# Optimization experiments

Measured on AMD Instinct MI355X. Metric: run time of the kernel, lower is better.

## Reference

```python
import jax, jax.numpy as jnp
import numpy as np

N_NODES = 50000
N_EDGES = 1250000
D = 64


def setup_inputs() -> dict:
    key = jax.random.key(0)
    ks = jax.random.split(key, 9)
    s = 1.0 / np.sqrt(D)
    return {
        "y": jax.random.normal(ks[0], (N_NODES, D), dtype=jnp.float32),
        "src": jax.random.randint(ks[1], (N_EDGES,), 0, N_NODES, dtype=jnp.int32),
        "dst": jax.random.randint(ks[2], (N_EDGES,), 0, N_NODES, dtype=jnp.int32),
        "W1": jax.random.normal(ks[3], (D, D), dtype=jnp.float32) * s,
        "b1": jnp.zeros((D,), dtype=jnp.float32),
        "W2": jax.random.normal(ks[4], (D, D), dtype=jnp.float32) * s,
        "b2": jnp.zeros((D,), dtype=jnp.float32),
        "U1": jax.random.normal(ks[5], (D, D), dtype=jnp.float32) * s,
        "c1": jnp.zeros((D,), dtype=jnp.float32),
        "U2": jax.random.normal(ks[6], (D, D), dtype=jnp.float32) * s,
        "c2": jnp.zeros((D,), dtype=jnp.float32),
    }


def reference(y, src, dst, W1, b1, W2, b2, U1, c1, U2, c2):
    # msg = relu(FNN_pre(y[src])) ; FNN = Linear -> ReLU -> Linear
    xs = y[src]                                        # [E, D] gather
    h1 = jax.nn.relu(xs @ W1 + b1)                     # [E, D]
    msg = jax.nn.relu(h1 @ W2 + b2)                    # [E, D]
    # z = segment-sum of messages at destination nodes
    z = jax.ops.segment_sum(msg, dst, num_segments=N_NODES)  # [N, D]
    # h = relu(FNN_update(z))
    h2 = jax.nn.relu(z @ U1 + c1)                      # [N, D]
    h = jax.nn.relu(h2 @ U2 + c2)                      # [N, D]
    return h
```

## Files before the change

### kernel.cpp

```cpp
#include <hip/hip_runtime.h>

#define D 64
#define CHUNK 4096
#define BSHIFT 8
#define CAP 8192

typedef unsigned int uint;
typedef unsigned short ushort;

using bf16x8 = __attribute__((ext_vector_type(8))) short;
using f32x4  = __attribute__((ext_vector_type(4))) float;

__device__ __forceinline__ uint f2bf(float f) {
    uint u = __float_as_uint(f);
    return (u + 0x7fffu + ((u >> 16) & 1u)) >> 16;
}
__device__ __forceinline__ uint pk2(float a, float b) {
    return f2bf(a) | (f2bf(b) << 16);
}

#define ACC8M(v, aE, aO, mk) do {                                              \
    aE[0] = fmaf(mk, __uint_as_float((v).x << 16), aE[0]);                     \
    aO[0] = fmaf(mk, __uint_as_float((v).x & 0xffff0000u), aO[0]);             \
    aE[1] = fmaf(mk, __uint_as_float((v).y << 16), aE[1]);                     \
    aO[1] = fmaf(mk, __uint_as_float((v).y & 0xffff0000u), aO[1]);             \
    aE[2] = fmaf(mk, __uint_as_float((v).z << 16), aE[2]);                     \
    aO[2] = fmaf(mk, __uint_as_float((v).z & 0xffff0000u), aO[2]);             \
    aE[3] = fmaf(mk, __uint_as_float((v).w << 16), aE[3]);                     \
    aO[3] = fmaf(mk, __uint_as_float((v).w & 0xffff0000u), aO[3]);             \
} while (0)

template <bool BF16IN>
__device__ __forceinline__ void mlp_tile(
    int tile, ushort (*Hs)[72],
    const float* __restrict__ Xf, const ushort* __restrict__ Xb, int xstride,
    const ushort* __restrict__ pkW1, const float* __restrict__ b1v,
    const ushort* __restrict__ pkW2, const float* __restrict__ b2v,
    ushort* __restrict__ out16, float* __restrict__ out32, int N, bool store)
{
    const int lane = threadIdx.x & 63;
    const int m = lane & 15;
    const int q = lane >> 4;

    bf16x8 w1f[4][2], w2f[4][2];
    #pragma unroll
    for (int t = 0; t < 4; ++t) {
        #pragma unroll
        for (int kf = 0; kf < 2; ++kf) {
            const int off = ((t * 2 + kf) * 64 + lane) << 3;
            w1f[t][kf] = *(const bf16x8*)(pkW1 + off);
            w2f[t][kf] = *(const bf16x8*)(pkW2 + off);
        }
    }

    const int rowbase = tile * 16;
    int r = rowbase + m;
    if (r >= N) r = N - 1;
    bf16x8 ax0, ax1;
    if (BF16IN) {
        const ushort* xr = Xb + (size_t)r * xstride + q * 8;
        ax0 = *(const bf16x8*)xr;
        ax1 = *(const bf16x8*)(xr + 32);
    } else {
        const float* xr = Xf + (size_t)r * xstride + q * 8;
        float4 x0 = *(const float4*)xr;
        float4 x1 = *(const float4*)(xr + 4);
        float4 x2 = *(const float4*)(xr + 32);
        float4 x3 = *(const float4*)(xr + 36);
        ax0[0]=(short)f2bf(x0.x); ax0[1]=(short)f2bf(x0.y);
        ax0[2]=(short)f2bf(x0.z); ax0[3]=(short)f2bf(x0.w);
        ax0[4]=(short)f2bf(x1.x); ax0[5]=(short)f2bf(x1.y);
        ax0[6]=(short)f2bf(x1.z); ax0[7]=(short)f2bf(x1.w);
        ax1[0]=(short)f2bf(x2.x); ax1[1]=(short)f2bf(x2.y);
        ax1[2]=(short)f2bf(x2.z); ax1[3]=(short)f2bf(x2.w);
        ax1[4]=(short)f2bf(x3.x); ax1[5]=(short)f2bf(x3.y);
        ax1[6]=(short)f2bf(x3.z); ax1[7]=(short)f2bf(x3.w);
    }

    const f32x4 zero4 = {0.f, 0.f, 0.f, 0.f};
    f32x4 acc[4];

    #pragma unroll
    for (int t = 0; t < 4; ++t) acc[t] = zero4;
    #pragma unroll
    for (int t = 0; t < 4; ++t) {
        acc[t] = __builtin_amdgcn_mfma_f32_16x16x32_bf16(ax0, w1f[t][0], acc[t], 0, 0, 0);
        acc[t] = __builtin_amdgcn_mfma_f32_16x16x32_bf16(ax1, w1f[t][1], acc[t], 0, 0, 0);
    }
    #pragma unroll
    for (int t = 0; t < 4; ++t) {
        const float bv = b1v[t * 16 + m];
        #pragma unroll
        for (int rg = 0; rg < 4; ++rg) {
            float hv = fmaxf(acc[t][rg] + bv, 0.f);
            Hs[q * 4 + rg][t * 16 + m] = (ushort)f2bf(hv);
        }
    }
    __syncthreads();

    bf16x8 ah0 = *(const bf16x8*)&Hs[m][q * 8];
    bf16x8 ah1 = *(const bf16x8*)&Hs[m][32 + q * 8];

    #pragma unroll
    for (int t = 0; t < 4; ++t) acc[t] = zero4;
    #pragma unroll
    for (int t = 0; t < 4; ++t) {
        acc[t] = __builtin_amdgcn_mfma_f32_16x16x32_bf16(ah0, w2f[t][0], acc[t], 0, 0, 0);
        acc[t] = __builtin_amdgcn_mfma_f32_16x16x32_bf16(ah1, w2f[t][1], acc[t], 0, 0, 0);
    }
    __syncthreads();
    if (store) {
        #pragma unroll
        for (int t = 0; t < 4; ++t) {
            const float bv = b2v[t * 16 + m];
            #pragma unroll
            for (int rg = 0; rg < 4; ++rg) {
                const int row = rowbase + q * 4 + rg;
                if (row < N) {
                    float ov = fmaxf(acc[t][rg] + bv, 0.f);
                    if (out16) out16[(size_t)row * D + t * 16 + m] = (ushort)f2bf(ov);
                    else       out32[(size_t)row * D + t * 16 + m] = ov;
                }
            }
        }
    }
}

__global__ __launch_bounds__(256) void kInit(
    int* __restrict__ cursor,
    const float* __restrict__ W1, const float* __restrict__ W2,
    const float* __restrict__ U1, const float* __restrict__ U2,
    ushort* __restrict__ pkAll)
{
    const int t = threadIdx.x;
    if (blockIdx.x == 0) {
        cursor[t] = 0;
        return;
    }
    const int mtx = blockIdx.x - 1;
    const float* W = (mtx == 0) ? W1 : (mtx == 1) ? W2 : (mtx == 2) ? U1 : U2;
    ushort* pk = pkAll + mtx * 4096;
    for (int v = t; v < 512; v += 256) {
        const int t_ = v >> 7;
        const int rem = v & 127;
        const int kf = rem >> 6;
        const int lane = rem & 63;
        const int q = lane >> 4, m = lane & 15;
        const int n = t_ * 16 + m;
        uint w[4];
        #pragma unroll
        for (int j2 = 0; j2 < 4; ++j2) {
            const int k = kf * 32 + q * 8 + 2 * j2;
            w[j2] = pk2(W[k * D + n], W[(k + 1) * D + n]);
        }
        uint4 vv = { w[0], w[1], w[2], w[3] };
        *(uint4*)(pk + (v << 3)) = vv;
    }
}

__global__ __launch_bounds__(256) void kPart_mlp1(
    const int* __restrict__ src, const int* __restrict__ dst,
    int* __restrict__ cursor, uint* __restrict__ packedG, int E, int NBA,
    const float* __restrict__ y, const ushort* __restrict__ pkAll,
    const float* __restrict__ b1, const float* __restrict__ b2,
    ushort* __restrict__ msg16, int N)
{
    __shared__ int lhist[256];
    __shared__ int lcur[256];
    __shared__ __align__(16) ushort Hs[4][16][72];
    const int t = threadIdx.x;

    if ((int)blockIdx.x < NBA) {
        lhist[t] = 0;
        __syncthreads();
        const int cbase = blockIdx.x * CHUNK;
        const int lim = min(CHUNK, E - cbase);
        if (lim == CHUNK) {
            const int4* sp = (const int4*)(src + cbase);
            const int4* dp = (const int4*)(dst + cbase);
            int4 s4[4], d4[4];
            #pragma unroll
            for (int g = 0; g < 4; ++g) { s4[g] = sp[g * 256 + t]; d4[g] = dp[g * 256 + t]; }
            #pragma unroll
            for (int g = 0; g < 4; ++g) {
                atomicAdd(&lhist[(uint)d4[g].x >> BSHIFT], 1);
                atomicAdd(&lhist[(uint)d4[g].y >> BSHIFT], 1);
                atomicAdd(&lhist[(uint)d4[g].z >> BSHIFT], 1);
                atomicAdd(&lhist[(uint)d4[g].w >> BSHIFT], 1);
            }
            __syncthreads();
            int c = lhist[t];
            int base = 0;
            if (c > 0) base = atomicAdd(&cursor[t], c);
            lcur[t] = t * CAP + base;
            __syncthreads();
            #pragma unroll
            for (int g = 0; g < 4; ++g) {
                int pos;
                pos = atomicAdd(&lcur[(uint)d4[g].x >> BSHIFT], 1);
                packedG[pos] = ((uint)(d4[g].x & 255) << 16) | (uint)s4[g].x;
                pos = atomicAdd(&lcur[(uint)d4[g].y >> BSHIFT], 1);
                packedG[pos] = ((uint)(d4[g].y & 255) << 16) | (uint)s4[g].y;
                pos = atomicAdd(&lcur[(uint)d4[g].z >> BSHIFT], 1);
                packedG[pos] = ((uint)(d4[g].z & 255) << 16) | (uint)s4[g].z;
                pos = atomicAdd(&lcur[(uint)d4[g].w >> BSHIFT], 1);
                packedG[pos] = ((uint)(d4[g].w & 255) << 16) | (uint)s4[g].w;
            }
        } else {
            for (int j = t; j < lim; j += 256)
                atomicAdd(&lhist[(uint)dst[cbase + j] >> BSHIFT], 1);
            __syncthreads();
            int c = lhist[t];
            int base = 0;
            if (c > 0) base = atomicAdd(&cursor[t], c);
            lcur[t] = t * CAP + base;
            __syncthreads();
            for (int j = t; j < lim; j += 256) {
                int s = src[cbase + j], d = dst[cbase + j];
                int pos = atomicAdd(&lcur[(uint)d >> BSHIFT], 1);
                packedG[pos] = ((uint)(d & 255) << 16) | (uint)s;
            }
        }
    } else {
        const int tile = (blockIdx.x - NBA) * 4 + (t >> 6);
        mlp_tile<false>(tile, Hs[t >> 6], y, nullptr, D,
                        pkAll + 0 * 4096, b1, pkAll + 1 * 4096, b2,
                        msg16, nullptr, N, true);
    }
}

__global__ __launch_bounds__(256) void kSort(
    const uint* __restrict__ packedG, const int* __restrict__ cursor,
    ushort* __restrict__ sortedG, int* __restrict__ offsets,
    int* __restrict__ ends, int N)
{
    __shared__ int scn[256];
    __shared__ int cnt[256];
    __shared__ int cur[256];
    __shared__ ushort srt[CAP];
    const int t = threadIdx.x;
    const int b = blockIdx.x;
    const int base = b * CAP;
    const int cn = cursor[b];

    cnt[t] = 0;
    __syncthreads();
    for (int i = t; i < cn; i += 256)
        atomicAdd(&cnt[packedG[base + i] >> 16], 1);
    __syncthreads();

    int c = cnt[t];
    int x = c; scn[t] = x; __syncthreads();
    #pragma unroll
    for (int off = 1; off < 256; off <<= 1) {
        int add = (t >= off) ? scn[t - off] : 0; __syncthreads();
        x += add; scn[t] = x; __syncthreads();
    }
    const int excl = x - c;
    const int node = b * 256 + t;
    if (node < N) {
        offsets[node] = base + excl;
        ends[node]    = base + excl + c;
    }
    cur[t] = excl;
    __syncthreads();
    for (int i = t; i < cn; i += 256) {
        uint e = packedG[base + i];
        int p = atomicAdd(&cur[e >> 16], 1);
        srt[p] = (ushort)(e & 0xffffu);
    }
    __syncthreads();
    for (int i = t; i < cn; i += 256)
        sortedG[base + i] = srt[i];
}

__global__ __launch_bounds__(256) void kGatherMlp2(
    const ushort* __restrict__ msg16,
    const int* __restrict__ offsets, const int* __restrict__ ends,
    const ushort* __restrict__ sortedG,
    const ushort* __restrict__ pkAll,
    const float* __restrict__ c1, const float* __restrict__ c2,
    float* __restrict__ out, int N)
{
    __shared__ __align__(16) ushort Zs[16][72];
    __shared__ __align__(16) ushort Hs[16][72];
    const int t = threadIdx.x;
    const int wv = t >> 6;
    const int lane = t & 63;
    const int sub = lane & 7;
    const int grp = (lane >> 3) & 3;
    const int half = lane >> 5;
    const int il = lane & 31;
    const int hbase = lane & 32;
    const ushort* mbase = msg16 + (sub << 3);
    const int tile = blockIdx.x;

    #pragma unroll
    for (int pass = 0; pass < 2; ++pass) {
        const int pairIdx = pass * 4 + wv;
        const int n = tile * 16 + 2 * pairIdx + half;
        const bool nvalid = n < N;
        int beg = 0, end = 0;
        if (nvalid) { beg = offsets[n]; end = ends[n]; }
        const int m = end - beg;
        const int m0 = __builtin_amdgcn_readfirstlane(m);
        const int m1 = __builtin_amdgcn_readlane(m, 32);
        const int mmax = max(m0, m1);

        float aE[4] = {0, 0, 0, 0}, aO[4] = {0, 0, 0, 0};

        for (int base = 0; base < mmax; base += 32) {
            int idxv = 0;
            if (base + il < m) idxv = (int)sortedG[beg + base + il];
            int sj[8];
            #pragma unroll
            for (int j = 0; j < 8; ++j)
                if (base + j * 4 < mmax)
                    sj[j] = __shfl(idxv, hbase + j * 4 + grp, 64);
            uint4 v[8];
            #pragma unroll
            for (int j = 0; j < 8; ++j)
                if (base + j * 4 < mmax)
                    v[j] = *(const uint4*)(mbase + ((size_t)sj[j] << 6));
            #pragma unroll
            for (int j = 0; j < 8; ++j)
                if (base + j * 4 < mmax) {
                    const float mk = (base + j * 4 + grp < m) ? 1.f : 0.f;
                    ACC8M(v[j], aE, aO, mk);
                }
        }

        #pragma unroll
        for (int d2 = 0; d2 < 4; ++d2) {
            aE[d2] += __shfl_xor(aE[d2], 8, 64);
            aO[d2] += __shfl_xor(aO[d2], 8, 64);
            aE[d2] += __shfl_xor(aE[d2], 16, 64);
            aO[d2] += __shfl_xor(aO[d2], 16, 64);
        }
        if (grp == 0) {
            uint4 pv;
            pv.x = pk2(aE[0], aO[0]);
            pv.y = pk2(aE[1], aO[1]);
            pv.z = pk2(aE[2], aO[2]);
            pv.w = pk2(aE[3], aO[3]);
            *(uint4*)&Zs[2 * pairIdx + half][sub << 3] = pv;
        }
    }
    __syncthreads();

    mlp_tile<true>(tile, Hs, nullptr, &Zs[0][0] - (size_t)tile * 16 * 72, 72,
                   pkAll + 2 * 4096, c1, pkAll + 3 * 4096, c2,
                   nullptr, out, N, wv == 0);
}

extern "C" void kernel_launch(void* const* d_in, const int* in_sizes, int n_in,
                              void* d_out, int out_size, void* d_ws, size_t ws_size,
                              hipStream_t stream) {
    const float* y  = (const float*)d_in[0];
    const int*  src = (const int*) d_in[1];
    const int*  dst = (const int*) d_in[2];
    const float* W1 = (const float*)d_in[3];
    const float* b1 = (const float*)d_in[4];
    const float* W2 = (const float*)d_in[5];
    const float* b2 = (const float*)d_in[6];
    const float* U1 = (const float*)d_in[7];
    const float* c1 = (const float*)d_in[8];
    const float* U2 = (const float*)d_in[9];
    const float* c2 = (const float*)d_in[10];

    const int N = in_sizes[0] / D;
    const int E = in_sizes[1];
    const int NBA   = (E + CHUNK - 1) / CHUNK;
    const int NBUCK = (N + 255) / 256;
    const int NT    = (N + 15) / 16;
    const int MB    = (NT + 3) / 4;

    char* ws = (char*)d_ws;
    auto al16 = [](size_t x) { return (x + 15) & ~15ull; };
    ushort* msg16   = (ushort*)ws;  ws += al16((size_t)N * D * 2);
    int*    offsets = (int*)ws;     ws += al16((size_t)N * 4);
    int*    ends    = (int*)ws;     ws += al16((size_t)N * 4);
    int*    cursor  = (int*)ws;     ws += al16(256 * 4);
    ushort* pkAll   = (ushort*)ws;  ws += al16(4 * 4096 * 2);
    uint*   packedG = (uint*)ws;    ws += al16((size_t)NBUCK * CAP * 4);
    ushort* sortedG = (ushort*)ws;  ws += al16((size_t)NBUCK * CAP * 2);

    kInit<<<5, 256, 0, stream>>>(cursor, W1, W2, U1, U2, pkAll);

    kPart_mlp1<<<NBA + MB, 256, 0, stream>>>(
        src, dst, cursor, packedG, E, NBA, y, pkAll, b1, b2, msg16, N);

    kSort<<<NBUCK, 256, 0, stream>>>(packedG, cursor, sortedG, offsets, ends, N);

    kGatherMlp2<<<NT, 256, 0, stream>>>(
        msg16, offsets, ends, sortedG, pkAll, c1, c2, (float*)d_out, N);
}
```

Measured before the change: 146.7 us.

## Split fused gather+MLP2 kernel into separate gather and MLP kernels

The fused segment-gather plus update-MLP kernel is split in two. A gather kernel writes a bf16 z buffer to global memory, with each wave handling one node pair and no block-level sync. A separate MLP kernel then runs four independent 16-row tiles per block. This removes the __syncthreads and the idle waves that only one of four waves used for the MLP, and it raises gather occupancy through launch bounds. The cost is an extra kernel launch and a round trip of z through global memory.

```diff
diff --git a/kernel.cpp b/kernel.cpp
--- a/kernel.cpp
+++ b/kernel.cpp
@@ -33,10 +33,10 @@
 template <bool BF16IN>
 __device__ __forceinline__ void mlp_tile(
     int tile, ushort (*Hs)[72],
-    const float* __restrict__ Xf, const ushort* __restrict__ Xb, int xstride,
+    const float* __restrict__ Xf, const ushort* __restrict__ Xb,
     const ushort* __restrict__ pkW1, const float* __restrict__ b1v,
     const ushort* __restrict__ pkW2, const float* __restrict__ b2v,
-    ushort* __restrict__ out16, float* __restrict__ out32, int N, bool store)
+    ushort* __restrict__ out16, float* __restrict__ out32, int N)
 {
     const int lane = threadIdx.x & 63;
     const int m = lane & 15;
@@ -58,11 +58,11 @@
     if (r >= N) r = N - 1;
     bf16x8 ax0, ax1;
     if (BF16IN) {
-        const ushort* xr = Xb + (size_t)r * xstride + q * 8;
+        const ushort* xr = Xb + (size_t)r * D + q * 8;
         ax0 = *(const bf16x8*)xr;
         ax1 = *(const bf16x8*)(xr + 32);
     } else {
-        const float* xr = Xf + (size_t)r * xstride + q * 8;
+        const float* xr = Xf + (size_t)r * D + q * 8;
         float4 x0 = *(const float4*)xr;
         float4 x1 = *(const float4*)(xr + 4);
         float4 x2 = *(const float4*)(xr + 32);
@@ -108,19 +108,16 @@
         acc[t] = __builtin_amdgcn_mfma_f32_16x16x32_bf16(ah0, w2f[t][0], acc[t], 0, 0, 0);
         acc[t] = __builtin_amdgcn_mfma_f32_16x16x32_bf16(ah1, w2f[t][1], acc[t], 0, 0, 0);
     }
-    __syncthreads();
-    if (store) {
-        #pragma unroll
-        for (int t = 0; t < 4; ++t) {
-            const float bv = b2v[t * 16 + m];
-            #pragma unroll
-            for (int rg = 0; rg < 4; ++rg) {
-                const int row = rowbase + q * 4 + rg;
-                if (row < N) {
-                    float ov = fmaxf(acc[t][rg] + bv, 0.f);
-                    if (out16) out16[(size_t)row * D + t * 16 + m] = (ushort)f2bf(ov);
-                    else       out32[(size_t)row * D + t * 16 + m] = ov;
-                }
+    #pragma unroll
+    for (int t = 0; t < 4; ++t) {
+        const float bv = b2v[t * 16 + m];
+        #pragma unroll
+        for (int rg = 0; rg < 4; ++rg) {
+            const int row = rowbase + q * 4 + rg;
+            if (row < N) {
+                float ov = fmaxf(acc[t][rg] + bv, 0.f);
+                if (out16) out16[(size_t)row * D + t * 16 + m] = (ushort)f2bf(ov);
+                else       out32[(size_t)row * D + t * 16 + m] = ov;
             }
         }
     }
@@ -223,9 +220,9 @@
         }
     } else {
         const int tile = (blockIdx.x - NBA) * 4 + (t >> 6);
-        mlp_tile<false>(tile, Hs[t >> 6], y, nullptr, D,
+        mlp_tile<false>(tile, Hs[t >> 6], y, nullptr,
                         pkAll + 0 * 4096, b1, pkAll + 1 * 4096, b2,
-                        msg16, nullptr, N, true);
+                        msg16, nullptr, N);
     }
 }
 
@@ -274,83 +271,81 @@
         sortedG[base + i] = srt[i];
 }
 
-__global__ __launch_bounds__(256) void kGatherMlp2(
+__global__ __launch_bounds__(256, 6) void k5_gather(
     const ushort* __restrict__ msg16,
     const int* __restrict__ offsets, const int* __restrict__ ends,
     const ushort* __restrict__ sortedG,
-    const ushort* __restrict__ pkAll,
-    const float* __restrict__ c1, const float* __restrict__ c2,
-    float* __restrict__ out, int N)
-{
-    __shared__ __align__(16) ushort Zs[16][72];
-    __shared__ __align__(16) ushort Hs[16][72];
-    const int t = threadIdx.x;
-    const int wv = t >> 6;
-    const int lane = t & 63;
+    ushort* __restrict__ z16, int n_nodes)
+{
+    const int lane = threadIdx.x & 63;
     const int sub = lane & 7;
     const int grp = (lane >> 3) & 3;
     const int half = lane >> 5;
     const int il = lane & 31;
     const int hbase = lane & 32;
+    const int p = blockIdx.x * 4 + (threadIdx.x >> 6);
+    if (p * 2 >= n_nodes) return;
     const ushort* mbase = msg16 + (sub << 3);
-    const int tile = blockIdx.x;
-
-    #pragma unroll
-    for (int pass = 0; pass < 2; ++pass) {
-        const int pairIdx = pass * 4 + wv;
-        const int n = tile * 16 + 2 * pairIdx + half;
-        const bool nvalid = n < N;
-        int beg = 0, end = 0;
-        if (nvalid) { beg = offsets[n]; end = ends[n]; }
-        const int m = end - beg;
-        const int m0 = __builtin_amdgcn_readfirstlane(m);
-        const int m1 = __builtin_amdgcn_readlane(m, 32);
-        const int mmax = max(m0, m1);
-
-        float aE[4] = {0, 0, 0, 0}, aO[4] = {0, 0, 0, 0};
-
-        for (int base = 0; base < mmax; base += 32) {
-            int idxv = 0;
-            if (base + il < m) idxv = (int)sortedG[beg + base + il];
-            int sj[8];
-            #pragma unroll
-            for (int j = 0; j < 8; ++j)
-                if (base + j * 4 < mmax)
-                    sj[j] = __shfl(idxv, hbase + j * 4 + grp, 64);
-            uint4 v[8];
-            #pragma unroll
-            for (int j = 0; j < 8; ++j)
-                if (base + j * 4 < mmax)
-                    v[j] = *(const uint4*)(mbase + ((size_t)sj[j] << 6));
-            #pragma unroll
-            for (int j = 0; j < 8; ++j)
-                if (base + j * 4 < mmax) {
-                    const float mk = (base + j * 4 + grp < m) ? 1.f : 0.f;
-                    ACC8M(v[j], aE, aO, mk);
-                }
-        }
-
-        #pragma unroll
-        for (int d2 = 0; d2 < 4; ++d2) {
-            aE[d2] += __shfl_xor(aE[d2], 8, 64);
-            aO[d2] += __shfl_xor(aO[d2], 8, 64);
-            aE[d2] += __shfl_xor(aE[d2], 16, 64);
-            aO[d2] += __shfl_xor(aO[d2], 16, 64);
-        }
-        if (grp == 0) {
-            uint4 pv;
-            pv.x = pk2(aE[0], aO[0]);
-            pv.y = pk2(aE[1], aO[1]);
-            pv.z = pk2(aE[2], aO[2]);
-            pv.w = pk2(aE[3], aO[3]);
-            *(uint4*)&Zs[2 * pairIdx + half][sub << 3] = pv;
-        }
-    }
-    __syncthreads();
-
-    mlp_tile<true>(tile, Hs, nullptr, &Zs[0][0] - (size_t)tile * 16 * 72, 72,
+
+    const int n = 2 * p + half;
+    const bool nvalid = n < n_nodes;
+    int beg = 0, end = 0;
+    if (nvalid) { beg = offsets[n]; end = ends[n]; }
+    const int m = end - beg;
+    const int m0 = __builtin_amdgcn_readfirstlane(m);
+    const int m1 = __builtin_amdgcn_readlane(m, 32);
+    const int mmax = max(m0, m1);
+
+    float aE[4] = {0, 0, 0, 0}, aO[4] = {0, 0, 0, 0};
+
+    for (int base = 0; base < mmax; base += 32) {
+        int idxv = 0;
+        if (base + il < m) idxv = (int)sortedG[beg + base + il];
+        int sj[8];
+        #pragma unroll
+        for (int j = 0; j < 8; ++j)
+            if (base + j * 4 < mmax)
+                sj[j] = __shfl(idxv, hbase + j * 4 + grp, 64);
+        uint4 v[8];
+        #pragma unroll
+        for (int j = 0; j < 8; ++j)
+            if (base + j * 4 < mmax)
+                v[j] = *(const uint4*)(mbase + ((size_t)sj[j] << 6));
+        #pragma unroll
+        for (int j = 0; j < 8; ++j)
+            if (base + j * 4 < mmax) {
+                const float mk = (base + j * 4 + grp < m) ? 1.f : 0.f;
+                ACC8M(v[j], aE, aO, mk);
+            }
+    }
+
+    #pragma unroll
+    for (int d2 = 0; d2 < 4; ++d2) {
+        aE[d2] += __shfl_xor(aE[d2], 8, 64);
+        aO[d2] += __shfl_xor(aO[d2], 8, 64);
+        aE[d2] += __shfl_xor(aE[d2], 16, 64);
+        aO[d2] += __shfl_xor(aO[d2], 16, 64);
+    }
+    if (grp == 0 && nvalid) {
+        uint4 pv;
+        pv.x = pk2(aE[0], aO[0]);
+        pv.y = pk2(aE[1], aO[1]);
+        pv.z = pk2(aE[2], aO[2]);
+        pv.w = pk2(aE[3], aO[3]);
+        *(uint4*)(z16 + (size_t)n * D + (sub << 3)) = pv;
+    }
+}
+
+__global__ __launch_bounds__(256) void k_mlp2(
+    const ushort* __restrict__ z16, const ushort* __restrict__ pkAll,
+    const float* __restrict__ c1, const float* __restrict__ c2,
+    float* __restrict__ out, int N)
+{
+    __shared__ __align__(16) ushort Hs[4][16][72];
+    const int tile = blockIdx.x * 4 + (threadIdx.x >> 6);
+    mlp_tile<true>(tile, Hs[threadIdx.x >> 6], nullptr, z16,
                    pkAll + 2 * 4096, c1, pkAll + 3 * 4096, c2,
-                   nullptr, out, N, wv == 0);
+                   nullptr, out, N);
 }
 
 extern "C" void kernel_launch(void* const* d_in, const int* in_sizes, int n_in,
@@ -374,6 +369,7 @@
     const int NBUCK = (N + 255) / 256;
     const int NT    = (N + 15) / 16;
     const int MB    = (NT + 3) / 4;
+    const int G5    = (N / 2 + 3) / 4;
 
     char* ws = (char*)d_ws;
     auto al16 = [](size_t x) { return (x + 15) & ~15ull; };
@@ -384,6 +380,7 @@
     ushort* pkAll   = (ushort*)ws;  ws += al16(4 * 4096 * 2);
     uint*   packedG = (uint*)ws;    ws += al16((size_t)NBUCK * CAP * 4);
     ushort* sortedG = (ushort*)ws;  ws += al16((size_t)NBUCK * CAP * 2);
+    ushort* z16     = (ushort*)ws;  ws += al16((size_t)N * D * 2);
 
     kInit<<<5, 256, 0, stream>>>(cursor, W1, W2, U1, U2, pkAll);
 
@@ -392,6 +389,7 @@
 
     kSort<<<NBUCK, 256, 0, stream>>>(packedG, cursor, sortedG, offsets, ends, N);
 
-    kGatherMlp2<<<NT, 256, 0, stream>>>(
-        msg16, offsets, ends, sortedG, pkAll, c1, c2, (float*)d_out, N);
-}
+    k5_gather<<<G5, 256, 0, stream>>>(msg16, offsets, ends, sortedG, z16, N);
+
+    k_mlp2<<<MB, 256, 0, stream>>>(z16, pkAll, c1, c2, (float*)d_out, N);
+}
```

Result: faster. 142.5 us (-2.9%).
